# Performance work log

Hardware: AMD Instinct MI355X
Metric: run time of the kernel (lower is better)

## Reference

```python
import jax, jax.numpy as jnp
import numpy as np

B, C, H, W = 32, 256, 64, 64
EPS = 1e-8  # clamp for cosine-similarity denominators


def setup_inputs() -> dict:
    key = jax.random.key(0)
    k1, k2, k3 = jax.random.split(key, 3)
    unmasked = jax.random.normal(k1, (B, C, H, W), dtype=jnp.float32)
    masked = jax.random.normal(k2, (B, C, H, W), dtype=jnp.float32)
    latent_mask = jax.random.randint(k3, (B, H, W), 0, 2, dtype=jnp.int32)
    return {
        "unmasked_latent_tensors": unmasked,
        "masked_latent_tensors": masked,
        "latent_mask": latent_mask,
    }


def reference(unmasked_latent_tensors, masked_latent_tensors, latent_mask):
    # Original torch code builds a full [B, B*H*W, H, W] cross-activation of a
    # cosine-similarity 1x1 conv (input vs. every masked position used as a
    # prototype), then gathers only the diagonal entries where batch index and
    # spatial position match. Mathematically that diagonal is just the
    # per-position cosine similarity along the channel axis, computed here
    # directly.
    u = unmasked_latent_tensors
    m = masked_latent_tensors
    num = jnp.sum(u * m, axis=1)                       # [B, H, W]
    u_norm = jnp.sqrt(jnp.sum(u * u, axis=1))          # [B, H, W]
    m_norm = jnp.sqrt(jnp.sum(m * m, axis=1))          # [B, H, W]
    sim = num / (jnp.maximum(u_norm, EPS) * jnp.maximum(m_norm, EPS))
    # masked=True: average similarity over mask==1 positions.
    mask_f = (latent_mask != 0).astype(sim.dtype)      # [B, H, W]
    return jnp.sum(sim * mask_f) / jnp.sum(mask_f)
```

## Files before the change

kernel.cpp:

```cpp
#include <hip/hip_runtime.h>


#define BB   32
#define CC   256
#define HH   64
#define WW   64
#define HWSZ (HH * WW)
#define NPOS (BB * HWSZ)
#define SIM_EPS 1e-8f

__global__ __launch_bounds__(256) void
sim_reduce_kernel(const float* __restrict__ u,
                  const float* __restrict__ m,
                  const int* __restrict__ mask,
                  double* __restrict__ ws)
{
    const int p  = blockIdx.x * 256 + threadIdx.x;
    const int b  = p >> 12;
    const int hw = p & (HWSZ - 1);

    const size_t base = (size_t)b * CC * HWSZ + hw;
    const float* up = u + base;
    const float* mp = m + base;

    float num = 0.f, uu = 0.f, mm = 0.f;
#pragma unroll 8
    for (int c = 0; c < CC; ++c) {
        const float a  = up[(size_t)c * HWSZ];
        const float bv = mp[(size_t)c * HWSZ];
        num = fmaf(a, bv, num);
        uu  = fmaf(a, a,  uu);
        mm  = fmaf(bv, bv, mm);
    }

    const float denom = fmaxf(sqrtf(uu), SIM_EPS) * fmaxf(sqrtf(mm), SIM_EPS);
    const float sim   = num / denom;

    const int mk = (mask[p] != 0) ? 1 : 0;
    double sd = mk ? (double)sim : 0.0;
    double md = (double)mk;

#pragma unroll
    for (int off = 32; off > 0; off >>= 1) {
        sd += __shfl_down(sd, off, 64);
        md += __shfl_down(md, off, 64);
    }

    __shared__ double lds_s[4];
    __shared__ double lds_m[4];
    const int wave = threadIdx.x >> 6;
    const int lane = threadIdx.x & 63;
    if (lane == 0) { lds_s[wave] = sd; lds_m[wave] = md; }
    __syncthreads();

    if (threadIdx.x == 0) {
        const double ts = lds_s[0] + lds_s[1] + lds_s[2] + lds_s[3];
        const double tm = lds_m[0] + lds_m[1] + lds_m[2] + lds_m[3];
        atomicAdd(&ws[0], ts);
        atomicAdd(&ws[1], tm);
    }
}

__global__ void finalize_kernel(const double* __restrict__ ws,
                                float* __restrict__ out)
{
    out[0] = (float)(ws[0] / ws[1]);
}

extern "C" void kernel_launch(void* const* d_in, const int* in_sizes, int n_in,
                              void* d_out, int out_size, void* d_ws, size_t ws_size,
                              hipStream_t stream)
{
    const float* u    = (const float*)d_in[0];
    const float* m    = (const float*)d_in[1];
    const int*   mask = (const int*)d_in[2];
    float*  out = (float*)d_out;
    double* ws  = (double*)d_ws;

    hipMemsetAsync(d_ws, 0, 2 * sizeof(double), stream);

    sim_reduce_kernel<<<NPOS / 256, 256, 0, stream>>>(u, m, mask, ws);
    finalize_kernel<<<1, 1, 0, stream>>>(ws, out);
}
```

Measured before the change: 279.7 us.

## Split channel reduction across threads with float4 loads and LDS combine

Each block now handles 128 positions, with 8 thread groups each reducing 32 channels for 4 adjacent positions using float4 loads. Partial sums are combined in shared memory before computing the cosine similarity and the masked reduction. This is meant to raise memory-level parallelism and shorten each thread's serial dependent load chain on a bandwidth-bound reduction. It costs an extra barrier and shared-memory traffic, and the summation order changes slightly.

```diff
diff --git a/kernel.cpp b/kernel.cpp
--- a/kernel.cpp
+++ b/kernel.cpp
@@ -1,44 +1,76 @@
 #include <hip/hip_runtime.h>
 
 
-#define BB   32
-#define CC   256
-#define HH   64
-#define WW   64
-#define HWSZ (HH * WW)
-#define NPOS (BB * HWSZ)
+#define BB    32
+#define CC    256
+#define HH    64
+#define WW    64
+#define HWSZ  (HH * WW)
+#define NPOS  (BB * HWSZ)
+#define CSPLIT 8
+#define CPER  (CC / CSPLIT)
+#define PGPB  32
+#define POSPB (PGPB * 4)
 #define SIM_EPS 1e-8f
 
-__global__ __launch_bounds__(256) void
+__global__ __launch_bounds__(256, 4) void
 sim_reduce_kernel(const float* __restrict__ u,
                   const float* __restrict__ m,
                   const int* __restrict__ mask,
                   double* __restrict__ ws)
 {
-    const int p  = blockIdx.x * 256 + threadIdx.x;
-    const int b  = p >> 12;
-    const int hw = p & (HWSZ - 1);
+    __shared__ float lds_num[CSPLIT * POSPB];
+    __shared__ float lds_uu [CSPLIT * POSPB];
+    __shared__ float lds_mm [CSPLIT * POSPB];
 
-    const size_t base = (size_t)b * CC * HWSZ + hw;
-    const float* up = u + base;
-    const float* mp = m + base;
+    const int tid    = threadIdx.x;
+    const int posgrp = tid & (PGPB - 1);
+    const int cchunk = tid >> 5;
 
-    float num = 0.f, uu = 0.f, mm = 0.f;
+    const int p0 = blockIdx.x * POSPB + posgrp * 4;
+    const int b  = p0 >> 12;
+    const int hw = p0 & (HWSZ - 1);
+
+    const size_t base = (size_t)b * CC * HWSZ + (size_t)cchunk * CPER * HWSZ + hw;
+    const float4* up = (const float4*)(u + base);
+    const float4* mp = (const float4*)(m + base);
+
+    float4 num = {0.f, 0.f, 0.f, 0.f};
+    float4 uu  = {0.f, 0.f, 0.f, 0.f};
+    float4 mm  = {0.f, 0.f, 0.f, 0.f};
+
 #pragma unroll 8
-    for (int c = 0; c < CC; ++c) {
-        const float a  = up[(size_t)c * HWSZ];
-        const float bv = mp[(size_t)c * HWSZ];
-        num = fmaf(a, bv, num);
-        uu  = fmaf(a, a,  uu);
-        mm  = fmaf(bv, bv, mm);
+    for (int c = 0; c < CPER; ++c) {
+        const float4 a = up[(size_t)c * (HWSZ / 4)];
+        const float4 v = mp[(size_t)c * (HWSZ / 4)];
+        num.x = fmaf(a.x, v.x, num.x); num.y = fmaf(a.y, v.y, num.y);
+        num.z = fmaf(a.z, v.z, num.z); num.w = fmaf(a.w, v.w, num.w);
+        uu.x  = fmaf(a.x, a.x, uu.x);  uu.y  = fmaf(a.y, a.y, uu.y);
+        uu.z  = fmaf(a.z, a.z, uu.z);  uu.w  = fmaf(a.w, a.w, uu.w);
+        mm.x  = fmaf(v.x, v.x, mm.x);  mm.y  = fmaf(v.y, v.y, mm.y);
+        mm.z  = fmaf(v.z, v.z, mm.z);  mm.w  = fmaf(v.w, v.w, mm.w);
     }
 
-    const float denom = fmaxf(sqrtf(uu), SIM_EPS) * fmaxf(sqrtf(mm), SIM_EPS);
-    const float sim   = num / denom;
+    ((float4*)lds_num)[cchunk * PGPB + posgrp] = num;
+    ((float4*)lds_uu )[cchunk * PGPB + posgrp] = uu;
+    ((float4*)lds_mm )[cchunk * PGPB + posgrp] = mm;
+    __syncthreads();
 
-    const int mk = (mask[p] != 0) ? 1 : 0;
-    double sd = mk ? (double)sim : 0.0;
-    double md = (double)mk;
+    double sd = 0.0, md = 0.0;
+    if (tid < POSPB) {
+        float n = 0.f, su = 0.f, sm = 0.f;
+#pragma unroll
+        for (int cc = 0; cc < CSPLIT; ++cc) {
+            n  += lds_num[cc * POSPB + tid];
+            su += lds_uu [cc * POSPB + tid];
+            sm += lds_mm [cc * POSPB + tid];
+        }
+        const float denom = fmaxf(sqrtf(su), SIM_EPS) * fmaxf(sqrtf(sm), SIM_EPS);
+        const float sim   = n / denom;
+        const int   mk    = (mask[blockIdx.x * POSPB + tid] != 0) ? 1 : 0;
+        sd = mk ? (double)sim : 0.0;
+        md = (double)mk;
+    }
 
 #pragma unroll
     for (int off = 32; off > 0; off >>= 1) {
@@ -46,16 +78,16 @@
         md += __shfl_down(md, off, 64);
     }
 
-    __shared__ double lds_s[4];
-    __shared__ double lds_m[4];
-    const int wave = threadIdx.x >> 6;
-    const int lane = threadIdx.x & 63;
-    if (lane == 0) { lds_s[wave] = sd; lds_m[wave] = md; }
+    __shared__ double red_s[4];
+    __shared__ double red_m[4];
+    const int wave = tid >> 6;
+    const int lane = tid & 63;
+    if (lane == 0) { red_s[wave] = sd; red_m[wave] = md; }
     __syncthreads();
 
-    if (threadIdx.x == 0) {
-        const double ts = lds_s[0] + lds_s[1] + lds_s[2] + lds_s[3];
-        const double tm = lds_m[0] + lds_m[1] + lds_m[2] + lds_m[3];
+    if (tid == 0) {
+        const double ts = red_s[0] + red_s[1] + red_s[2] + red_s[3];
+        const double tm = red_m[0] + red_m[1] + red_m[2] + red_m[3];
         atomicAdd(&ws[0], ts);
         atomicAdd(&ws[1], tm);
     }
@@ -79,6 +111,6 @@
 
     hipMemsetAsync(d_ws, 0, 2 * sizeof(double), stream);
 
-    sim_reduce_kernel<<<NPOS / 256, 256, 0, stream>>>(u, m, mask, ws);
+    sim_reduce_kernel<<<NPOS / POSPB, 256, 0, stream>>>(u, m, mask, ws);
     finalize_kernel<<<1, 1, 0, stream>>>(ws, out);
 }
```

Result: no change. 284.1 us (+1.6%).
